# Optimization experiments

Measured on AMD Instinct MI355X. Metric: run time of the kernel, lower is better.

Reference implementation:

```python
import jax, jax.numpy as jnp
import numpy as np

FS = 512.0
SEQ_LEN = 2048
PHA_N, AMP_N, N_BINS = 50, 30, 18


def _bands():
    # PAC.calc_bands_pha: mid in linspace(2,20,50), band = [mid - mid/4, mid + mid/4]
    pha_mid = np.linspace(2.0, 20.0, PHA_N)
    pha = np.stack([pha_mid * 0.75, pha_mid * 1.25], axis=1)
    # amp_end_hz = int(min(fs/2/(1+0.8) - 1, 160)) = 141 for fs=512
    amp_end = float(int(min(FS / 2.0 / 1.8 - 1.0, 160.0)))
    # PAC.calc_bands_amp: mid in linspace(60,141,30), band = [mid - mid/8, mid + mid/8]
    amp_mid = np.linspace(60.0, amp_end, AMP_N)
    amp = np.stack([amp_mid * 0.875, amp_mid * 1.125], axis=1)
    return np.concatenate([pha, amp], axis=0).astype(np.float32)  # (80, 2)


def setup_inputs() -> dict:
    key = jax.random.key(0)
    x = jax.random.normal(key, (2, 8, 1, SEQ_LEN), dtype=jnp.float32)
    return {"x": x}


def _pac(x):
    # x: (B, C, S, T)
    B, C, S, T = x.shape
    bands = jnp.asarray(_bands())                        # (F, 2), F = 80
    freqs = jnp.abs(jnp.fft.fftfreq(T, d=1.0 / FS)).astype(jnp.float32)
    # zero-phase brick-wall bandpass masks, one per band
    mask = ((freqs[None, :] >= bands[:, :1]) & (freqs[None, :] <= bands[:, 1:2])).astype(jnp.complex64)  # (F, T)
    # Hilbert analytic-signal multiplier (T even)
    half = T // 2
    h = jnp.zeros((T,), jnp.float32).at[0].set(1.0).at[half].set(1.0).at[1:half].set(2.0)
    Xf = jnp.fft.fft(x, axis=-1)                          # (B, C, S, T) complex
    analytic = jnp.fft.ifft(Xf[:, :, :, None, :] * mask[None, None, None] * h.astype(jnp.complex64), axis=-1)  # (B, C, S, F, T)
    # transpose segments/bands as in forward (x.transpose(2, 3))
    pha = jnp.angle(analytic).transpose(0, 1, 3, 2, 4)[:, :, :PHA_N]   # (B, C, P, S, T)
    amp = jnp.abs(analytic).transpose(0, 1, 3, 2, 4)[:, :, -AMP_N:]    # (B, C, A, S, T)
    edge = T // 8
    pha = pha[..., edge:-edge]
    amp = amp[..., edge:-edge]                                          # Tt = T - 2*edge
    # Modulation index: bin phases into 18 bins over [-pi, pi], mean amp per bin
    width = 2.0 * jnp.pi / N_BINS
    idx = jnp.clip(jnp.floor((pha + jnp.pi) / width), 0, N_BINS - 1).astype(jnp.int32)
    oh = jax.nn.one_hot(idx, N_BINS, dtype=amp.dtype)                   # (B, C, P, S, Tt, K)
    counts = oh.sum(axis=-2)                                            # (B, C, P, S, K)
    sums = jnp.einsum('bcpstk,bcast->bcpask', oh, amp)                  # (B, C, P, A, S, K)
    means = sums / jnp.maximum(counts[:, :, :, None], 1e-9)
    probs = means / jnp.maximum(means.sum(axis=-1, keepdims=True), 1e-9)
    log_nb = jnp.log(jnp.float32(N_BINS))
    # MI = (log K + sum_k p log p) / log K  (KL divergence from uniform, normalized)
    mi = (log_nb + (probs * jnp.log(probs + 1e-9)).sum(axis=-1)) / log_nb  # (B, C, P, A, S)
    return mi.mean(axis=-1)                                             # (B, C, P, A)


def reference(x):
    return _pac(x)
```

## Files before the change

kernel.cpp:

```cpp
#include <hip/hip_runtime.h>
#include <hip/hip_bf16.h>
#include <math.h>

#ifndef M_PI
#define M_PI 3.14159265358979323846
#endif

#define T 2048
#define EDGE 256
#define TT 1536
#define PHA_N 50
#define AMP_N 30
#define NBANDS 80
#define NBINS 18
#define NBC 16
#define FMAX 768
#define NCH 16
#define CHLEN (T / NCH)
#define BK 640
#define BWAVES 4
#define KPW (BK / BWAVES)

typedef __attribute__((ext_vector_type(8))) short short8;
typedef __attribute__((ext_vector_type(8))) _Float16 half8;
typedef __attribute__((ext_vector_type(16))) float float16;

__device__ __forceinline__ void band_range(int band, int* fl, int* fh) {
    double lo, hi;
    if (band < PHA_N) {
        double mid = 2.0 + (double)band * (18.0 / 49.0);
        lo = (double)(float)(mid * 0.75);
        hi = (double)(float)(mid * 1.25);
    } else {
        int j = band - PHA_N;
        double mid = 60.0 + (double)j * (81.0 / 29.0);
        lo = (double)(float)(mid * 0.875);
        hi = (double)(float)(mid * 1.125);
    }
    int l = (int)ceil(lo * 4.0);
    int h = (int)floor(hi * 4.0);
    if (l < 1) l = 1;
    if (h > FMAX - 1) h = FMAX - 1;
    *fl = l; *fh = h;
}

__global__ void dft_kernel(const float* __restrict__ x, float2* __restrict__ Xp) {
    __shared__ float xs[CHLEN];
    const int bc = blockIdx.x;
    const int fb = blockIdx.y;
    const int ch = blockIdx.z;
    const int tid = threadIdx.x;
    const int t0 = ch * CHLEN;
    if (tid < CHLEN) xs[tid] = x[bc * T + t0 + tid];
    __syncthreads();
    const int f = fb * 256 + tid;
    const float omf = (float)(2.0 * M_PI / (double)T);
    float s, c;
    sincosf(omf * (float)(f & (T - 1)), &s, &c);
    const float wR = c, wI = -s;
    float curR[2], curI[2], accR[2], accI[2];
    #pragma unroll
    for (int h = 0; h < 2; ++h) {
        sincosf(omf * (float)((f * (t0 + h * 64)) & (T - 1)), &s, &c);
        curR[h] = c; curI[h] = -s;
        accR[h] = 0.0f; accI[h] = 0.0f;
    }
    #pragma unroll 2
    for (int t = 0; t < 64; ++t) {
        #pragma unroll
        for (int h = 0; h < 2; ++h) {
            const float v = xs[t + h * 64];
            accR[h] += v * curR[h];
            accI[h] += v * curI[h];
            const float nR = curR[h] * wR - curI[h] * wI;
            const float nI = curR[h] * wI + curI[h] * wR;
            curR[h] = nR; curI[h] = nI;
        }
    }
    Xp[(size_t)((ch * NBC + bc) * FMAX + f)] =
        make_float2(accR[0] + accR[1], accI[0] + accI[1]);
}

__global__ void reduce_kernel(const float2* __restrict__ Xp, float2* __restrict__ Xf) {
    const int gid = blockIdx.x * 256 + threadIdx.x;
    float r = 0.0f, im = 0.0f;
    #pragma unroll
    for (int c = 0; c < NCH; ++c) {
        const float2 v = Xp[(size_t)c * NBC * FMAX + gid];
        r += v.x; im += v.y;
    }
    Xf[gid] = make_float2(r, im);
}

__global__ __launch_bounds__(256, 3)
void band_kernel(const float2* __restrict__ Xf,
                 unsigned char* __restrict__ idx_buf,
                 _Float16* __restrict__ Abuf) {
    __shared__ float uni[2560];
    __shared__ float cpart[BWAVES][2560];
    __shared__ int bfl_s[96], bfh_s[96];
    const int bc = blockIdx.x;
    const int tg = blockIdx.y;
    const int tid = threadIdx.x;
    const int wave = tid >> 6, lane = tid & 63;
    const int n = lane & 31;
    const int kq = lane >> 5;
    const int t = tg * 32 + n + EDGE;

    for (int i = tid; i < BK; i += 256) {
        const float2 v = Xf[bc * FMAX + i + 1];
        uni[i] = v.x; uni[1280 + i] = v.y;
    }
    if (tid < 96) {
        int fl = 1, fh = 0;
        if (tid < NBANDS) band_range(tid, &fl, &fh);
        bfl_s[tid] = fl; bfh_s[tid] = fh;
    }
    __syncthreads();

    const int fl0 = bfl_s[n],      fh0 = bfh_s[n];
    const int fl1 = bfl_s[32 + n], fh1 = bfh_s[32 + n];
    const int fl2 = bfl_s[64 + n], fh2 = bfh_s[64 + n];

    const float omf = (float)(2.0 * M_PI / (double)T);
    float sw, cw;
    sincosf(omf * (float)(t & (T - 1)), &sw, &cw);
    float r16c = cw, r16s = sw;
    #pragma unroll
    for (int q = 0; q < 4; ++q) {
        const float nc = r16c * r16c - r16s * r16s;
        const float ns = 2.0f * r16c * r16s;
        r16c = nc; r16s = ns;
    }
    const int Koff = wave * KPW;
    const int gg0 = 1 + Koff + kq * 8;
    float cur0c, cur0s;
    { float s0, c0; sincosf(omf * (float)((gg0 * t) & (T - 1)), &s0, &c0);
      cur0c = c0; cur0s = s0; }

    float16 aR0 = {0.0f}, aR1 = {0.0f}, aR2 = {0.0f};
    float16 aI0 = {0.0f}, aI1 = {0.0f}, aI2 = {0.0f};
    for (int ks = 0; ks < 10; ++ks) {
        const int kbase = Koff + kq * 8 + ks * 16;
        float cc = cur0c, cs = cur0s;
        half8 bre, bim;
        #pragma unroll
        for (int j = 0; j < 8; ++j) {
            const float Xr = uni[kbase + j];
            const float Xi = uni[1280 + kbase + j];
            bre[j] = (_Float16)(Xr * cc - Xi * cs);
            bim[j] = (_Float16)(Xr * cs + Xi * cc);
            const float nc = cc * cw - cs * sw;
            const float ns = cc * sw + cs * cw;
            cc = nc; cs = ns;
        }
        { const float nc = cur0c * r16c - cur0s * r16s;
          const float ns = cur0c * r16s + cur0s * r16c;
          cur0c = nc; cur0s = ns; }
        short8 a0s, a1s, a2s;
        #pragma unroll
        for (int j = 0; j < 8; ++j) {
            const int g = kbase + j + 1;
            a0s[j] = (g >= fl0 && g <= fh0) ? (short)0x3C00 : (short)0;
            a1s[j] = (g >= fl1 && g <= fh1) ? (short)0x3C00 : (short)0;
            a2s[j] = (g >= fl2 && g <= fh2) ? (short)0x3C00 : (short)0;
        }
        const half8 a0 = __builtin_bit_cast(half8, a0s);
        const half8 a1 = __builtin_bit_cast(half8, a1s);
        const half8 a2 = __builtin_bit_cast(half8, a2s);
        aR0 = __builtin_amdgcn_mfma_f32_32x32x16_f16(a0, bre, aR0, 0, 0, 0);
        aI0 = __builtin_amdgcn_mfma_f32_32x32x16_f16(a0, bim, aI0, 0, 0, 0);
        aR1 = __builtin_amdgcn_mfma_f32_32x32x16_f16(a1, bre, aR1, 0, 0, 0);
        aI1 = __builtin_amdgcn_mfma_f32_32x32x16_f16(a1, bim, aI1, 0, 0, 0);
        aR2 = __builtin_amdgcn_mfma_f32_32x32x16_f16(a2, bre, aR2, 0, 0, 0);
        aI2 = __builtin_amdgcn_mfma_f32_32x32x16_f16(a2, bim, aI2, 0, 0, 0);
    }
    __syncthreads();

    #pragma unroll
    for (int r = 0; r < 16; ++r) {
        const int row = (r & 3) + 8 * (r >> 2) + 4 * kq;
        cpart[wave][row * 32 + n] = aR0[r];
        cpart[wave][(32 + row) * 32 + n] = aR1[r];
        if (row < 16) cpart[wave][(64 + row) * 32 + n] = aR2[r];
    }
    __syncthreads();
    for (int i = tid; i < 2560; i += 256)
        uni[i] = cpart[0][i] + cpart[1][i] + cpart[2][i] + cpart[3][i];
    __syncthreads();
    #pragma unroll
    for (int r = 0; r < 16; ++r) {
        const int row = (r & 3) + 8 * (r >> 2) + 4 * kq;
        cpart[wave][row * 32 + n] = aI0[r];
        cpart[wave][(32 + row) * 32 + n] = aI1[r];
        if (row < 16) cpart[wave][(64 + row) * 32 + n] = aI2[r];
    }
    __syncthreads();

    const float widthf = (float)(2.0 * M_PI / (double)NBINS);
    const float pif = (float)M_PI;
    for (int i = tid; i < 2560; i += 256) {
        const int band = i >> 5, nn = i & 31;
        const float Sre = uni[i];
        const float Sim = cpart[0][i] + cpart[1][i] + cpart[2][i] + cpart[3][i];
        const int trel = tg * 32 + nn;
        if (band < PHA_N) {
            float pha = atan2f(Sim, Sre);
            int b = (int)floorf((pha + pif) / widthf);
            if (b < 0) b = 0;
            if (b > NBINS - 1) b = NBINS - 1;
            idx_buf[(size_t)(bc * PHA_N + band) * TT + trel] = (unsigned char)b;
        } else {
            float amp = sqrtf(Sre * Sre + Sim * Sim) * (2.0f / (float)T);
            Abuf[(size_t)(bc * 32 + (band - PHA_N)) * TT + trel] = (_Float16)amp;
        }
    }
    if (tid < 32)
        Abuf[(size_t)(bc * 32 + 30) * TT + tg * 32 + tid] = (_Float16)1.0f;
}

__global__ void mi_kernel(const unsigned char* __restrict__ idx_buf,
                          const _Float16* __restrict__ Abuf,
                          float* __restrict__ out) {
    __shared__ unsigned int sidx_s[TT / 4];
    __shared__ float cpart[4][32][NBINS];
    const int blk = blockIdx.x;
    const int bc = blk / PHA_N;
    const int p = blk % PHA_N;
    const int tid = threadIdx.x;
    const int wave = tid >> 6;
    const int lane = tid & 63;

    for (int i = tid; i < TT / 4; i += 256)
        sidx_s[i] = ((const unsigned int*)(idx_buf + (size_t)(bc * PHA_N + p) * TT))[i];
    __syncthreads();

    const int n = lane & 31;
    const int kq = lane >> 5;
    const half8* arow = (const half8*)(Abuf + (size_t)(bc * 32 + n) * TT
                                       + wave * 384 + kq * 8);
    float16 acc = {0.0f};
    #pragma unroll 4
    for (int ks = 0; ks < 24; ++ks) {
        const half8 a = arow[ks * 2];
        const int w0 = wave * 96 + ks * 4 + kq * 2;
        const unsigned int lo = sidx_s[w0];
        const unsigned int hi = sidx_s[w0 + 1];
        short8 bs;
        bs[0] = ((lo & 0xffu) == (unsigned)n) ? (short)0x3C00 : (short)0;
        bs[1] = (((lo >> 8) & 0xffu) == (unsigned)n) ? (short)0x3C00 : (short)0;
        bs[2] = (((lo >> 16) & 0xffu) == (unsigned)n) ? (short)0x3C00 : (short)0;
        bs[3] = ((lo >> 24) == (unsigned)n) ? (short)0x3C00 : (short)0;
        bs[4] = ((hi & 0xffu) == (unsigned)n) ? (short)0x3C00 : (short)0;
        bs[5] = (((hi >> 8) & 0xffu) == (unsigned)n) ? (short)0x3C00 : (short)0;
        bs[6] = (((hi >> 16) & 0xffu) == (unsigned)n) ? (short)0x3C00 : (short)0;
        bs[7] = ((hi >> 24) == (unsigned)n) ? (short)0x3C00 : (short)0;
        const half8 b = __builtin_bit_cast(half8, bs);
        acc = __builtin_amdgcn_mfma_f32_32x32x16_f16(a, b, acc, 0, 0, 0);
    }

    if (n < NBINS) {
        #pragma unroll
        for (int r = 0; r < 16; ++r) {
            const int row = (r & 3) + 8 * (r >> 2) + 4 * kq;
            if (row < 31) cpart[wave][row][n] = acc[r];
        }
    }
    __syncthreads();

    if (tid < AMP_N) {
        const int a = tid;
        float m[NBINS], tot = 0.0f;
        #pragma unroll
        for (int k = 0; k < NBINS; ++k) {
            const float cnt = cpart[0][30][k] + cpart[1][30][k]
                            + cpart[2][30][k] + cpart[3][30][k];
            const float denom = cnt > 1e-9f ? cnt : 1e-9f;
            const float s = cpart[0][a][k] + cpart[1][a][k]
                          + cpart[2][a][k] + cpart[3][a][k];
            m[k] = s / denom;
            tot += m[k];
        }
        const float dt = tot > 1e-9f ? tot : 1e-9f;
        float accm = 0.0f;
        #pragma unroll
        for (int k = 0; k < NBINS; ++k) {
            const float pr = m[k] / dt;
            accm += pr * logf(pr + 1e-9f);
        }
        const float lognb = 2.8903717578961645f;
        out[(size_t)blk * AMP_N + a] = (lognb + accm) / lognb;
    }
}

extern "C" void kernel_launch(void* const* d_in, const int* in_sizes, int n_in,
                              void* d_out, int out_size, void* d_ws, size_t ws_size,
                              hipStream_t stream) {
    const float* x = (const float*)d_in[0];
    float* out = (float*)d_out;
    char* ws = (char*)d_ws;
    unsigned char* idx_buf = (unsigned char*)ws;
    _Float16* Abuf = (_Float16*)(ws + 1228800);
    float2* Xp = (float2*)(ws + 2801664);
    float2* Xf = (float2*)(ws + 4374528);

    dft_kernel<<<dim3(NBC, FMAX / 256, NCH), 256, 0, stream>>>(x, Xp);
    reduce_kernel<<<NBC * FMAX / 256, 256, 0, stream>>>(Xp, Xf);
    band_kernel<<<dim3(NBC, TT / 32), 256, 0, stream>>>(Xf, idx_buf, Abuf);
    mi_kernel<<<NBC * PHA_N, 256, 0, stream>>>(idx_buf, Abuf, out);
}
```

Baseline: 98.04 us.

## Fuse partial-DFT reduction into band kernel and skip empty MFMA k-blocks

Removes the separate reduce kernel. Each band_kernel block now sums the 16 channel partials itself while loading its spectrum into shared memory, which saves one launch and a global round trip. It also computes per-tile frequency ranges for the three band groups and skips the twiddle generation and MFMAs for 16-wide k-blocks that fall outside every band in a group. The cost is redundant partial summation across the 48 time-tile blocks per channel, plus divergent branching around the MFMAs, which are wave-uniform here.

After: 99.62 us. No clear change (+1.6%).

```diff
diff --git a/kernel.cpp b/kernel.cpp
--- a/kernel.cpp
+++ b/kernel.cpp
@@ -81,19 +81,8 @@
         make_float2(accR[0] + accR[1], accI[0] + accI[1]);
 }
 
-__global__ void reduce_kernel(const float2* __restrict__ Xp, float2* __restrict__ Xf) {
-    const int gid = blockIdx.x * 256 + threadIdx.x;
-    float r = 0.0f, im = 0.0f;
-    #pragma unroll
-    for (int c = 0; c < NCH; ++c) {
-        const float2 v = Xp[(size_t)c * NBC * FMAX + gid];
-        r += v.x; im += v.y;
-    }
-    Xf[gid] = make_float2(r, im);
-}
-
 __global__ __launch_bounds__(256, 3)
-void band_kernel(const float2* __restrict__ Xf,
+void band_kernel(const float2* __restrict__ Xp,
                  unsigned char* __restrict__ idx_buf,
                  _Float16* __restrict__ Abuf) {
     __shared__ float uni[2560];
@@ -108,8 +97,14 @@
     const int t = tg * 32 + n + EDGE;
 
     for (int i = tid; i < BK; i += 256) {
-        const float2 v = Xf[bc * FMAX + i + 1];
-        uni[i] = v.x; uni[1280 + i] = v.y;
+        const int f = i + 1;
+        float r = 0.0f, im = 0.0f;
+        #pragma unroll
+        for (int c = 0; c < NCH; ++c) {
+            const float2 v = Xp[(size_t)(c * NBC + bc) * FMAX + f];
+            r += v.x; im += v.y;
+        }
+        uni[i] = r; uni[1280 + i] = im;
     }
     if (tid < 96) {
         int fl = 1, fh = 0;
@@ -121,6 +116,17 @@
     const int fl0 = bfl_s[n],      fh0 = bfh_s[n];
     const int fl1 = bfl_s[32 + n], fh1 = bfh_s[32 + n];
     const int fl2 = bfl_s[64 + n], fh2 = bfh_s[64 + n];
+
+    int gmin[3] = {100000, 100000, 100000}, gmax[3] = {0, 0, 0};
+    #pragma unroll
+    for (int tau = 0; tau < 3; ++tau)
+        for (int i = 0; i < 32; ++i) {
+            const int fl = bfl_s[tau * 32 + i], fh = bfh_s[tau * 32 + i];
+            if (fl <= fh) {
+                gmin[tau] = min(gmin[tau], fl);
+                gmax[tau] = max(gmax[tau], fh);
+            }
+        }
 
     const float omf = (float)(2.0 * M_PI / (double)T);
     float sw, cw;
@@ -141,39 +147,62 @@
     float16 aR0 = {0.0f}, aR1 = {0.0f}, aR2 = {0.0f};
     float16 aI0 = {0.0f}, aI1 = {0.0f}, aI2 = {0.0f};
     for (int ks = 0; ks < 10; ++ks) {
-        const int kbase = Koff + kq * 8 + ks * 16;
-        float cc = cur0c, cs = cur0s;
-        half8 bre, bim;
-        #pragma unroll
-        for (int j = 0; j < 8; ++j) {
-            const float Xr = uni[kbase + j];
-            const float Xi = uni[1280 + kbase + j];
-            bre[j] = (_Float16)(Xr * cc - Xi * cs);
-            bim[j] = (_Float16)(Xr * cs + Xi * cc);
-            const float nc = cc * cw - cs * sw;
-            const float ns = cc * sw + cs * cw;
-            cc = nc; cs = ns;
+        const int kb0 = Koff + ks * 16;
+        const int glo = kb0 + 1, ghi = kb0 + 16;
+        const bool act0 = (ghi >= gmin[0]) && (glo <= gmax[0]);
+        const bool act1 = (ghi >= gmin[1]) && (glo <= gmax[1]);
+        const bool act2 = (ghi >= gmin[2]) && (glo <= gmax[2]);
+        if (act0 || act1 || act2) {
+            const int kbase = kb0 + kq * 8;
+            float cc = cur0c, cs = cur0s;
+            half8 bre, bim;
+            #pragma unroll
+            for (int j = 0; j < 8; ++j) {
+                const float Xr = uni[kbase + j];
+                const float Xi = uni[1280 + kbase + j];
+                bre[j] = (_Float16)(Xr * cc - Xi * cs);
+                bim[j] = (_Float16)(Xr * cs + Xi * cc);
+                const float nc = cc * cw - cs * sw;
+                const float ns = cc * sw + cs * cw;
+                cc = nc; cs = ns;
+            }
+            if (act0) {
+                short8 as;
+                #pragma unroll
+                for (int j = 0; j < 8; ++j) {
+                    const int g = kbase + j + 1;
+                    as[j] = (g >= fl0 && g <= fh0) ? (short)0x3C00 : (short)0;
+                }
+                const half8 a = __builtin_bit_cast(half8, as);
+                aR0 = __builtin_amdgcn_mfma_f32_32x32x16_f16(a, bre, aR0, 0, 0, 0);
+                aI0 = __builtin_amdgcn_mfma_f32_32x32x16_f16(a, bim, aI0, 0, 0, 0);
+            }
+            if (act1) {
+                short8 as;
+                #pragma unroll
+                for (int j = 0; j < 8; ++j) {
+                    const int g = kbase + j + 1;
+                    as[j] = (g >= fl1 && g <= fh1) ? (short)0x3C00 : (short)0;
+                }
+                const half8 a = __builtin_bit_cast(half8, as);
+                aR1 = __builtin_amdgcn_mfma_f32_32x32x16_f16(a, bre, aR1, 0, 0, 0);
+                aI1 = __builtin_amdgcn_mfma_f32_32x32x16_f16(a, bim, aI1, 0, 0, 0);
+            }
+            if (act2) {
+                short8 as;
+                #pragma unroll
+                for (int j = 0; j < 8; ++j) {
+                    const int g = kbase + j + 1;
+                    as[j] = (g >= fl2 && g <= fh2) ? (short)0x3C00 : (short)0;
+                }
+                const half8 a = __builtin_bit_cast(half8, as);
+                aR2 = __builtin_amdgcn_mfma_f32_32x32x16_f16(a, bre, aR2, 0, 0, 0);
+                aI2 = __builtin_amdgcn_mfma_f32_32x32x16_f16(a, bim, aI2, 0, 0, 0);
+            }
         }
         { const float nc = cur0c * r16c - cur0s * r16s;
           const float ns = cur0c * r16s + cur0s * r16c;
           cur0c = nc; cur0s = ns; }
-        short8 a0s, a1s, a2s;
-        #pragma unroll
-        for (int j = 0; j < 8; ++j) {
-            const int g = kbase + j + 1;
-            a0s[j] = (g >= fl0 && g <= fh0) ? (short)0x3C00 : (short)0;
-            a1s[j] = (g >= fl1 && g <= fh1) ? (short)0x3C00 : (short)0;
-            a2s[j] = (g >= fl2 && g <= fh2) ? (short)0x3C00 : (short)0;
-        }
-        const half8 a0 = __builtin_bit_cast(half8, a0s);
-        const half8 a1 = __builtin_bit_cast(half8, a1s);
-        const half8 a2 = __builtin_bit_cast(half8, a2s);
-        aR0 = __builtin_amdgcn_mfma_f32_32x32x16_f16(a0, bre, aR0, 0, 0, 0);
-        aI0 = __builtin_amdgcn_mfma_f32_32x32x16_f16(a0, bim, aI0, 0, 0, 0);
-        aR1 = __builtin_amdgcn_mfma_f32_32x32x16_f16(a1, bre, aR1, 0, 0, 0);
-        aI1 = __builtin_amdgcn_mfma_f32_32x32x16_f16(a1, bim, aI1, 0, 0, 0);
-        aR2 = __builtin_amdgcn_mfma_f32_32x32x16_f16(a2, bre, aR2, 0, 0, 0);
-        aI2 = __builtin_amdgcn_mfma_f32_32x32x16_f16(a2, bim, aI2, 0, 0, 0);
     }
     __syncthreads();
 
@@ -302,10 +331,8 @@
     unsigned char* idx_buf = (unsigned char*)ws;
     _Float16* Abuf = (_Float16*)(ws + 1228800);
     float2* Xp = (float2*)(ws + 2801664);
-    float2* Xf = (float2*)(ws + 4374528);
 
     dft_kernel<<<dim3(NBC, FMAX / 256, NCH), 256, 0, stream>>>(x, Xp);
-    reduce_kernel<<<NBC * FMAX / 256, 256, 0, stream>>>(Xp, Xf);
-    band_kernel<<<dim3(NBC, TT / 32), 256, 0, stream>>>(Xf, idx_buf, Abuf);
+    band_kernel<<<dim3(NBC, TT / 32), 256, 0, stream>>>(Xp, idx_buf, Abuf);
     mi_kernel<<<NBC * PHA_N, 256, 0, stream>>>(idx_buf, Abuf, out);
 }
```
